# Performance work log

Hardware: AMD Instinct MI355X
Metric: run time of the kernel (lower is better)

The kernel has to match this reference:

```python
import jax, jax.numpy as jnp
import numpy as np

NEG_SLOPE = 0.2  # GAT LeakyReLU slope
NEG_INF = -1e9


def setup_inputs() -> dict:
    key = jax.random.key(0)
    ks = jax.random.split(key, 5)
    B, N, D = 16, 1024, 256
    H, F = 4, 64  # heads, per-head out dim (out_dim=256)
    x = jax.random.normal(ks[0], (B, N, D), dtype=jnp.float32)
    adj = jax.random.uniform(ks[1], (B, N, N), dtype=jnp.float32)
    W = jax.random.normal(ks[2], (D, H * F), dtype=jnp.float32) * (1.0 / np.sqrt(D))
    a_src = jax.random.normal(ks[3], (H, F), dtype=jnp.float32) * (1.0 / np.sqrt(F))
    a_dst = jax.random.normal(ks[4], (H, F), dtype=jnp.float32) * (1.0 / np.sqrt(F))
    bias = jnp.zeros((H * F,), dtype=jnp.float32)
    return {"x": x, "adj": adj, "W": W, "a_src": a_src, "a_dst": a_dst, "bias": bias}


def reference(x, adj, W, a_src, a_dst, bias):
    B, N, D = x.shape
    H, F = a_src.shape
    # Linear transform per head: [B,N,H,F]
    h = jnp.einsum("bnd,dhf->bnhf", x, W.reshape(D, H, F))
    # Attention logit components: [B,N,H]
    e_src = jnp.einsum("bnhf,hf->bnh", h, a_src)
    e_dst = jnp.einsum("bnhf,hf->bnh", h, a_dst)
    # logits[b,i,j,h]: target i gathers from source j (edge = adj[b,i,j] > 0.5)
    logits = e_dst[:, :, None, :] + e_src[:, None, :, :]
    logits = jnp.where(logits >= 0, logits, NEG_SLOPE * logits)  # LeakyReLU
    mask = adj > 0.5  # [B,N,N]
    logits = jnp.where(mask[..., None], logits, NEG_INF)
    att = jax.nn.softmax(logits, axis=2)  # softmax over source neighbors j
    out = jnp.einsum("bijh,bjhf->bihf", att, h)  # aggregate
    return out.reshape(B, N, H * F) + bias  # concat heads
```

## Files before the change

### kernel.cpp

```cpp
#include <hip/hip_runtime.h>

typedef __bf16 bf16x8 __attribute__((ext_vector_type(8)));
typedef float f32x4 __attribute__((ext_vector_type(4)));

constexpr int Bsz = 16;
constexpr int Nsz = 1024;
constexpr int Dsz = 256;
constexpr int Hsz = 4;
constexpr int HFsz = 256;
constexpr int BN = Bsz * Nsz;

__device__ __forceinline__ unsigned f2bf(float f) {
    unsigned u = __float_as_uint(f);
    return (u + 0x7FFFu + ((u >> 16) & 1u)) >> 16;
}

__global__ __launch_bounds__(256) void wcvt(const float* __restrict__ Wm,
                                            unsigned short* __restrict__ WbT) {
    const int t = threadIdx.x;
    const int c = blockIdx.x * 4 + (t >> 6);
    const int d0 = (t & 63) * 4;
    const float v0 = Wm[(size_t)(d0 + 0) * HFsz + c];
    const float v1 = Wm[(size_t)(d0 + 1) * HFsz + c];
    const float v2 = Wm[(size_t)(d0 + 2) * HFsz + c];
    const float v3 = Wm[(size_t)(d0 + 3) * HFsz + c];
    uint2 pk;
    pk.x = f2bf(v0) | (f2bf(v1) << 16);
    pk.y = f2bf(v2) | (f2bf(v3) << 16);
    *(uint2*)&WbT[(size_t)c * Dsz + d0] = pk;
}

__global__ __launch_bounds__(256) void gat_h_e3(
    const float* __restrict__ x,
    const unsigned short* __restrict__ WbT,
    const float* __restrict__ a_src,
    const float* __restrict__ a_dst,
    unsigned short* __restrict__ hT,
    float* __restrict__ esrcT,
    float* __restrict__ edstT)
{
    const int n0g = blockIdx.x * 32, b = n0g >> 10, n0 = n0g & 1023;
    const int t = threadIdx.x, lane = t & 63, w = t >> 6;
    const int m = lane & 15, q = lane >> 4;

    __shared__ alignas(16) unsigned short Lds[4 * 64 * 40];

    const float4* x4 = (const float4*)(x + (size_t)n0g * Dsz);
#pragma unroll
    for (int i = 0; i < 8; ++i) {
        const int f = t + 256 * i;
        const int row = f >> 6, d4 = (f & 63) * 4;
        const float4 xv = x4[f];
        uint2 pk;
        pk.x = f2bf(xv.x) | (f2bf(xv.y) << 16);
        pk.y = f2bf(xv.z) | (f2bf(xv.w) << 16);
        *(uint2*)&Lds[row * 264 + d4] = pk;
    }
    __syncthreads();

    const unsigned short* Ab = WbT + (size_t)(w * 64 + m) * Dsz + q * 8;
    f32x4 acc[4][2];
#pragma unroll
    for (int ht = 0; ht < 4; ++ht)
#pragma unroll
        for (int nt = 0; nt < 2; ++nt) acc[ht][nt] = (f32x4){0.f, 0.f, 0.f, 0.f};

#pragma unroll
    for (int kk = 0; kk < 8; ++kk) {
        const int k0 = kk * 32;
        const bf16x8 bfr0 = *(const bf16x8*)&Lds[(0 * 16 + m) * 264 + k0 + q * 8];
        const bf16x8 bfr1 = *(const bf16x8*)&Lds[(1 * 16 + m) * 264 + k0 + q * 8];
#pragma unroll
        for (int ht = 0; ht < 4; ++ht) {
            const bf16x8 afr = *(const bf16x8*)&Ab[ht * 16 * Dsz + k0];
            acc[ht][0] = __builtin_amdgcn_mfma_f32_16x16x32_bf16(afr, bfr0, acc[ht][0], 0, 0, 0);
            acc[ht][1] = __builtin_amdgcn_mfma_f32_16x16x32_bf16(afr, bfr1, acc[ht][1], 0, 0, 0);
        }
    }

    float ps0 = 0.f, ps1 = 0.f, pd0 = 0.f, pd1 = 0.f;
#pragma unroll
    for (int ht = 0; ht < 4; ++ht)
#pragma unroll
        for (int r = 0; r < 4; ++r) {
            const float as = a_src[w * 64 + ht * 16 + q * 4 + r];
            const float ad = a_dst[w * 64 + ht * 16 + q * 4 + r];
            ps0 += acc[ht][0][r] * as;  ps1 += acc[ht][1][r] * as;
            pd0 += acc[ht][0][r] * ad;  pd1 += acc[ht][1][r] * ad;
        }
    ps0 += __shfl_xor(ps0, 16, 64); ps0 += __shfl_xor(ps0, 32, 64);
    ps1 += __shfl_xor(ps1, 16, 64); ps1 += __shfl_xor(ps1, 32, 64);
    pd0 += __shfl_xor(pd0, 16, 64); pd0 += __shfl_xor(pd0, 32, 64);
    pd1 += __shfl_xor(pd1, 16, 64); pd1 += __shfl_xor(pd1, 32, 64);
    if (q == 0) {
        const size_t eb = (size_t)(b * Hsz + w) * Nsz + n0;
        esrcT[eb + m] = ps0;  esrcT[eb + 16 + m] = ps1;
        edstT[eb + m] = pd0;  edstT[eb + 16 + m] = pd1;
    }

    __syncthreads();

#pragma unroll
    for (int ht = 0; ht < 4; ++ht)
#pragma unroll
        for (int r = 0; r < 4; ++r) {
            const int hf = ht * 16 + q * 4 + r;
            Lds[w * 2560 + hf * 40 + m]      = (unsigned short)f2bf(acc[ht][0][r]);
            Lds[w * 2560 + hf * 40 + 16 + m] = (unsigned short)f2bf(acc[ht][1][r]);
        }
#pragma unroll
    for (int s = 0; s < 4; ++s) {
        const int hf = s * 16 + (lane >> 2), ck = lane & 3;
        const bf16x8 hv = *(const bf16x8*)&Lds[w * 2560 + hf * 40 + ck * 8];
        *(bf16x8*)&hT[(size_t)(b * HFsz + w * 64 + hf) * Nsz + n0 + ck * 8] = hv;
    }
}

__global__ __launch_bounds__(64) void gat_attn4(
    const float* __restrict__ adj,
    const unsigned short* __restrict__ hT,
    const float* __restrict__ esrcT,
    const float* __restrict__ edstT,
    const float* __restrict__ bias,
    float* __restrict__ outp)
{
    const int gid = blockIdx.x;
    const int b  = gid & 15;
    const int w  = (gid >> 4) & 3;
    const int i0 = (gid >> 6) * 16;
    const int lane = threadIdx.x, m = lane & 15, q = lane >> 4;

    __shared__ alignas(16) unsigned short P_s[16][72];
    __shared__ alignas(16) float ots[16][68];

    const float* adjb = adj + (size_t)b * Nsz * Nsz + (size_t)i0 * Nsz;
    const float* esb  = esrcT + (size_t)(b * Hsz + w) * Nsz;
    const float* edb  = edstT + (size_t)(b * Hsz + w) * Nsz + i0;
    const unsigned short* hTb = hT + (size_t)(b * HFsz + w * 64 + m) * Nsz + q * 8;

    float edreg[16];
#pragma unroll
    for (int il = 0; il < 16; ++il) edreg[il] = edb[il];

    bf16x8 ones;
#pragma unroll
    for (int i = 0; i < 8; ++i)
        ((unsigned short*)&ones)[i] = 0x3F80;

    float aA[16], aB[16];
    float esA, esB;
#pragma unroll
    for (int il = 0; il < 16; ++il) aA[il] = adjb[(size_t)il * Nsz + lane];
    esA = esb[lane];

    f32x4 acc[4];
#pragma unroll
    for (int nt = 0; nt < 4; ++nt) acc[nt] = (f32x4){0.f, 0.f, 0.f, 0.f};
    f32x4 acc5 = (f32x4){0.f, 0.f, 0.f, 0.f};

    auto body = [&](int jt, float (&ac)[16], float& esc,
                    float (&an)[16], float& esn) {
        const int j0 = jt * 64;
        bf16x8 bfr[8];
#pragma unroll
        for (int kk = 0; kk < 2; ++kk)
#pragma unroll
            for (int nt = 0; nt < 4; ++nt)
                bfr[kk * 4 + nt] =
                    *(const bf16x8*)&hTb[(size_t)nt * 16 * Nsz + j0 + kk * 32];

        const int jn = (jt < 15) ? j0 + 64 : j0;
#pragma unroll
        for (int il = 0; il < 16; ++il)
            an[il] = adjb[(size_t)il * Nsz + jn + lane];
        esn = esb[jn + lane];

#pragma unroll
        for (int il = 0; il < 16; ++il) {
            float v = edreg[il] + esc;
            v = fmaxf(v, 0.2f * v);
            const float p = __expf(v);
            unsigned u = __float_as_uint(p);
            u = (ac[il] > 0.5f) ? u : 0u;
            P_s[il][lane] = (unsigned short)(u >> 16);
        }
#pragma unroll
        for (int kk = 0; kk < 2; ++kk) {
            const bf16x8 afrag = *(const bf16x8*)&P_s[m][kk * 32 + q * 8];
#pragma unroll
            for (int nt = 0; nt < 4; ++nt)
                acc[nt] = __builtin_amdgcn_mfma_f32_16x16x32_bf16(
                    afrag, bfr[kk * 4 + nt], acc[nt], 0, 0, 0);
            acc5 = __builtin_amdgcn_mfma_f32_16x16x32_bf16(afrag, ones, acc5,
                                                           0, 0, 0);
        }
    };

    for (int jt = 0; jt < 16; jt += 2) {
        body(jt, aA, esA, aB, esB);
        body(jt + 1, aB, esB, aA, esA);
    }

    float linv[4];
#pragma unroll
    for (int r = 0; r < 4; ++r) linv[r] = 1.f / acc5[r];

#pragma unroll
    for (int nt = 0; nt < 4; ++nt)
#pragma unroll
        for (int r = 0; r < 4; ++r)
            ots[q * 4 + r][nt * 16 + m] = acc[nt][r] * linv[r];

    const float4 bias4 = *(const float4*)&bias[w * 64 + m * 4];
#pragma unroll
    for (int s = 0; s < 4; ++s) {
        const int row = s * 4 + q;
        float4 v = *(const float4*)&ots[row][m * 4];
        v.x += bias4.x; v.y += bias4.y; v.z += bias4.z; v.w += bias4.w;
        *(float4*)&outp[(size_t)(b * Nsz + i0 + row) * HFsz + w * 64 + m * 4] = v;
    }
}

extern "C" void kernel_launch(void* const* d_in, const int* in_sizes, int n_in,
                              void* d_out, int out_size, void* d_ws, size_t ws_size,
                              hipStream_t stream) {
    const float* x     = (const float*)d_in[0];
    const float* adj   = (const float*)d_in[1];
    const float* Wm    = (const float*)d_in[2];
    const float* a_src = (const float*)d_in[3];
    const float* a_dst = (const float*)d_in[4];
    const float* bias  = (const float*)d_in[5];
    float* outp = (float*)d_out;

    unsigned short* hT  = (unsigned short*)d_ws;
    unsigned short* WbT = hT + (size_t)BN * HFsz;
    float* esrcT = (float*)(WbT + (size_t)HFsz * Dsz);
    float* edstT = esrcT + (size_t)Bsz * Hsz * Nsz;

    wcvt<<<dim3(64), dim3(256), 0, stream>>>(Wm, WbT);
    gat_h_e3<<<dim3(BN / 32), dim3(256), 0, stream>>>(x, WbT, a_src, a_dst,
                                                      hT, esrcT, edstT);
    gat_attn4<<<dim3(4096), dim3(64), 0, stream>>>(adj, hT, esrcT, edstT,
                                                   bias, outp);
}
```

Before: 185.6 us.

## Split attention key loop across four waves per block with LDS reduction

```diff
diff --git a/kernel.cpp b/kernel.cpp
--- a/kernel.cpp
+++ b/kernel.cpp
@@ -116,7 +116,7 @@
     }
 }
 
-__global__ __launch_bounds__(64) void gat_attn4(
+__global__ __launch_bounds__(256, 8) void gat_attn5(
     const float* __restrict__ adj,
     const unsigned short* __restrict__ hT,
     const float* __restrict__ esrcT,
@@ -126,39 +126,44 @@
 {
     const int gid = blockIdx.x;
     const int b  = gid & 15;
-    const int w  = (gid >> 4) & 3;
+    const int hw = (gid >> 4) & 3;
     const int i0 = (gid >> 6) * 16;
-    const int lane = threadIdx.x, m = lane & 15, q = lane >> 4;
-
-    __shared__ alignas(16) unsigned short P_s[16][72];
-    __shared__ alignas(16) float ots[16][68];
+    const int t = threadIdx.x;
+    const int lane = t & 63, ws = t >> 6;
+    const int m = lane & 15, q = lane >> 4;
+
+    __shared__ alignas(16) unsigned char smem[20480];
+    unsigned short* Pw = (unsigned short*)smem + ws * 1152;
 
     const float* adjb = adj + (size_t)b * Nsz * Nsz + (size_t)i0 * Nsz;
-    const float* esb  = esrcT + (size_t)(b * Hsz + w) * Nsz;
-    const float* edb  = edstT + (size_t)(b * Hsz + w) * Nsz + i0;
-    const unsigned short* hTb = hT + (size_t)(b * HFsz + w * 64 + m) * Nsz + q * 8;
-
+    const float* esb  = esrcT + (size_t)(b * Hsz + hw) * Nsz;
+    const float* edb  = edstT + (size_t)(b * Hsz + hw) * Nsz + i0;
+    const unsigned short* hTb = hT + (size_t)(b * HFsz + hw * 64 + m) * Nsz + q * 8;
+
+    constexpr float LOG2E = 1.44269504088896340736f;
     float edreg[16];
 #pragma unroll
-    for (int il = 0; il < 16; ++il) edreg[il] = edb[il];
+    for (int il = 0; il < 16; ++il) edreg[il] = edb[il] * LOG2E;
 
     bf16x8 ones;
 #pragma unroll
     for (int i = 0; i < 8; ++i)
         ((unsigned short*)&ones)[i] = 0x3F80;
 
+    const int jbase = ws * 4;
+
     float aA[16], aB[16];
     float esA, esB;
 #pragma unroll
-    for (int il = 0; il < 16; ++il) aA[il] = adjb[(size_t)il * Nsz + lane];
-    esA = esb[lane];
+    for (int il = 0; il < 16; ++il) aA[il] = adjb[(size_t)il * Nsz + jbase * 64 + lane];
+    esA = esb[jbase * 64 + lane] * LOG2E;
 
     f32x4 acc[4];
 #pragma unroll
     for (int nt = 0; nt < 4; ++nt) acc[nt] = (f32x4){0.f, 0.f, 0.f, 0.f};
     f32x4 acc5 = (f32x4){0.f, 0.f, 0.f, 0.f};
 
-    auto body = [&](int jt, float (&ac)[16], float& esc,
+    auto body = [&](int jt, int jn, float (&ac)[16], float& esc,
                     float (&an)[16], float& esn) {
         const int j0 = jt * 64;
         bf16x8 bfr[8];
@@ -169,24 +174,24 @@
                 bfr[kk * 4 + nt] =
                     *(const bf16x8*)&hTb[(size_t)nt * 16 * Nsz + j0 + kk * 32];
 
-        const int jn = (jt < 15) ? j0 + 64 : j0;
 #pragma unroll
         for (int il = 0; il < 16; ++il)
             an[il] = adjb[(size_t)il * Nsz + jn + lane];
-        esn = esb[jn + lane];
+        esn = esb[jn + lane] * LOG2E;
 
 #pragma unroll
         for (int il = 0; il < 16; ++il) {
             float v = edreg[il] + esc;
             v = fmaxf(v, 0.2f * v);
-            const float p = __expf(v);
+            float p;
+            asm("v_exp_f32 %0, %1" : "=v"(p) : "v"(v));
             unsigned u = __float_as_uint(p);
             u = (ac[il] > 0.5f) ? u : 0u;
-            P_s[il][lane] = (unsigned short)(u >> 16);
+            Pw[il * 72 + lane] = (unsigned short)(u >> 16);
         }
 #pragma unroll
         for (int kk = 0; kk < 2; ++kk) {
-            const bf16x8 afrag = *(const bf16x8*)&P_s[m][kk * 32 + q * 8];
+            const bf16x8 afrag = *(const bf16x8*)&Pw[m * 72 + kk * 32 + q * 8];
 #pragma unroll
             for (int nt = 0; nt < 4; ++nt)
                 acc[nt] = __builtin_amdgcn_mfma_f32_16x16x32_bf16(
@@ -196,29 +201,44 @@
         }
     };
 
-    for (int jt = 0; jt < 16; jt += 2) {
-        body(jt, aA, esA, aB, esB);
-        body(jt + 1, aB, esB, aA, esA);
-    }
-
-    float linv[4];
-#pragma unroll
-    for (int r = 0; r < 4; ++r) linv[r] = 1.f / acc5[r];
-
-#pragma unroll
-    for (int nt = 0; nt < 4; ++nt)
-#pragma unroll
-        for (int r = 0; r < 4; ++r)
-            ots[q * 4 + r][nt * 16 + m] = acc[nt][r] * linv[r];
-
-    const float4 bias4 = *(const float4*)&bias[w * 64 + m * 4];
-#pragma unroll
-    for (int s = 0; s < 4; ++s) {
-        const int row = s * 4 + q;
-        float4 v = *(const float4*)&ots[row][m * 4];
-        v.x += bias4.x; v.y += bias4.y; v.z += bias4.z; v.w += bias4.w;
-        *(float4*)&outp[(size_t)(b * Nsz + i0 + row) * HFsz + w * 64 + m * 4] = v;
-    }
+    body(jbase + 0, (jbase + 1) * 64, aA, esA, aB, esB);
+    body(jbase + 1, (jbase + 2) * 64, aB, esB, aA, esA);
+    body(jbase + 2, (jbase + 3) * 64, aA, esA, aB, esB);
+    body(jbase + 3, (jbase + 3) * 64, aB, esB, aA, esA);
+
+    __syncthreads();
+    float* comb = (float*)smem;
+    {
+        float* cw = comb + (ws * 64 + lane) * 20;
+#pragma unroll
+        for (int nt = 0; nt < 4; ++nt)
+#pragma unroll
+            for (int r = 0; r < 4; ++r) cw[nt * 4 + r] = acc[nt][r];
+#pragma unroll
+        for (int r = 0; r < 4; ++r) cw[16 + r] = acc5[r];
+    }
+    __syncthreads();
+
+    const int row = t >> 4, c4 = t & 15;
+    const int rq = row >> 2, rr = row & 3;
+    const int nt4 = (c4 >> 2) * 4;
+    const int mb = (c4 & 3) * 4;
+    float n0 = 0.f, n1 = 0.f, n2 = 0.f, n3 = 0.f, den = 0.f;
+#pragma unroll
+    for (int w4 = 0; w4 < 4; ++w4) {
+        const float* cb = comb + (w4 * 64 + rq * 16) * 20;
+        den += cb[16 + rr];
+        n0 += cb[(mb + 0) * 20 + nt4 + rr];
+        n1 += cb[(mb + 1) * 20 + nt4 + rr];
+        n2 += cb[(mb + 2) * 20 + nt4 + rr];
+        n3 += cb[(mb + 3) * 20 + nt4 + rr];
+    }
+    const float inv = 1.f / den;
+    const float4 b4 = *(const float4*)&bias[hw * 64 + c4 * 4];
+    float4 o;
+    o.x = n0 * inv + b4.x;  o.y = n1 * inv + b4.y;
+    o.z = n2 * inv + b4.z;  o.w = n3 * inv + b4.w;
+    *(float4*)&outp[(size_t)(b * Nsz + i0 + row) * HFsz + hw * 64 + c4 * 4] = o;
 }
 
 extern "C" void kernel_launch(void* const* d_in, const int* in_sizes, int n_in,
@@ -240,6 +260,6 @@
     wcvt<<<dim3(64), dim3(256), 0, stream>>>(Wm, WbT);
     gat_h_e3<<<dim3(BN / 32), dim3(256), 0, stream>>>(x, WbT, a_src, a_dst,
                                                       hT, esrcT, edstT);
-    gat_attn4<<<dim3(4096), dim3(64), 0, stream>>>(adj, hT, esrcT, edstT,
-                                                   bias, outp);
-}
+    gat_attn5<<<dim3(4096), dim3(256), 0, stream>>>(adj, hT, esrcT, edstT,
+                                                    bias, outp);
+}
```

New measurement: 333.1 us. 79.4% more time.
